# Kernel optimization log

Measured on AMD Instinct MI355X. Metric: run time of the kernel, lower is better.

## Reference

```python
import jax, jax.numpy as jnp
import numpy as np

B, L, E, H = 8192, 64, 128, 8  # batch, max seq len, info_size, head_num
HD = E // H                    # head dim


def setup_inputs() -> dict:
    key = jax.random.key(0)
    k1, k2, k3, k4, k5, k6 = jax.random.split(key, 6)
    inter_info = jax.random.normal(k1, (B, L, E), dtype=jnp.float32)
    # ragged lengths in [1, L] (each sample has at least the query vector)
    lengths = jax.random.randint(k2, (B,), 1, L + 1, dtype=jnp.int32)
    s = 1.0 / np.sqrt(E)
    in_proj_w = jax.random.uniform(k3, (3 * E, E), dtype=jnp.float32, minval=-s, maxval=s)
    in_proj_b = jnp.zeros((3 * E,), dtype=jnp.float32)
    out_proj_w = jax.random.uniform(k4, (E, E), dtype=jnp.float32, minval=-s, maxval=s)
    out_proj_b = jnp.zeros((E,), dtype=jnp.float32)
    return {"inter_info": inter_info, "lengths": lengths,
            "in_proj_w": in_proj_w, "in_proj_b": in_proj_b,
            "out_proj_w": out_proj_w, "out_proj_b": out_proj_b}


def reference(inter_info, lengths, in_proj_w, in_proj_b, out_proj_w, out_proj_b):
    # Per sample: query = first vector, keys/values = all (valid) vectors.
    # Equivalent to torch nn.MultiheadAttention with 1 query per sample.
    Wq, Wk, Wv = in_proj_w[:E], in_proj_w[E:2 * E], in_proj_w[2 * E:]
    bq, bk, bv = in_proj_b[:E], in_proj_b[E:2 * E], in_proj_b[2 * E:]

    query_info = inter_info[:, 0]                                  # [B, E]
    q = (query_info @ Wq.T + bq).reshape(B, H, HD)                 # [B, H, hd]
    k = (inter_info @ Wk.T + bk).reshape(B, L, H, HD)              # [B, L, H, hd]
    v = (inter_info @ Wv.T + bv).reshape(B, L, H, HD)

    scores = jnp.einsum('bhd,blhd->bhl', q, k) / np.sqrt(HD)       # [B, H, L]
    valid = jnp.arange(L)[None, :] < lengths[:, None]              # [B, L]
    scores = jnp.where(valid[:, None, :], scores, -jnp.inf)
    attn = jax.nn.softmax(scores, axis=-1)                         # [B, H, L]

    ctx = jnp.einsum('bhl,blhd->bhd', attn, v).reshape(B, E)       # [B, E]
    attn_hidden = ctx @ out_proj_w.T + out_proj_b                  # [B, E]
    return attn_hidden, query_info
```

## Files before the change

### kernel.cpp

```cpp
#include <hip/hip_runtime.h>
#include <hip/hip_bf16.h>


typedef unsigned int  u32;
typedef unsigned short u16;
typedef unsigned long long u64;

#define XR  136
#define XR4 17
#define YR  136
#define UR  136
#define SCR 68
#define QR  132
#define YSR 1032

#define WS_U_OFF 0u
#define WS_C_OFF 16777216u
#define WS_Y_OFF 17825792u
#define WS_NEED  34603008u

typedef __attribute__((ext_vector_type(8))) __bf16 bf16x8;
typedef __attribute__((ext_vector_type(4))) float  f32x4;

__device__ __forceinline__ float blo(u32 u) { return __uint_as_float(u << 16); }
__device__ __forceinline__ float bhi(u32 u) { return __uint_as_float(u & 0xffff0000u); }
__device__ __forceinline__ float b2f(u16 u) { return __uint_as_float(((u32)u) << 16); }
__device__ __forceinline__ u16 f2b(float f) {
  union { __hip_bfloat16 h; u16 u; } cv; cv.h = __float2bfloat16(f); return cv.u;
}
__device__ __forceinline__ u32 pack2(float a, float b) {
  return (u32)f2b(a) | ((u32)f2b(b) << 16);
}

template<bool BF>
__device__ __forceinline__ uint4 wfrag(const void* p, size_t off) {
  if (BF) {
    return *(const uint4*)((const u16*)p + off);
  } else {
    const float4* q4 = (const float4*)((const float*)p + off);
    float4 a = q4[0], b = q4[1];
    uint4 v;
    v.x = pack2(a.x, a.y); v.y = pack2(a.z, a.w);
    v.z = pack2(b.x, b.y); v.w = pack2(b.z, b.w);
    return v;
  }
}
template<bool BF>
__device__ __forceinline__ void load4(const void* p, size_t off, float* o) {
  if (BF) {
    uint2 v = *(const uint2*)((const u16*)p + off);
    o[0]=blo(v.x); o[1]=bhi(v.x); o[2]=blo(v.y); o[3]=bhi(v.y);
  } else {
    float4 v = *(const float4*)((const float*)p + off);
    o[0]=v.x; o[1]=v.y; o[2]=v.z; o[3]=v.w;
  }
}
template<bool BF>
__device__ __forceinline__ float lds1(const void* p, size_t off) {
  return BF ? b2f(((const u16*)p)[off]) : ((const float*)p)[off];
}

struct __align__(16) SmemK1 {
  u16   X0s[8 * XR];
  float q[8 * QR];
  int   isbf;
};

template<bool BF>
__device__ __forceinline__ void k1_body(SmemK1& S, int b0, int t,
    const void* inter, const void* w_in, const void* b_in,
    u16* Uws, float* Cws)
{
  const int lane = t & 63, w = t >> 6;

  if (t < 128) {
    const int i = t >> 4, ci = t & 15;
    const size_t bidx = (size_t)(b0 + i);
    uint4 v;
    if (BF) {
      v = ((const uint4*)inter)[bidx * 1024 + ci];
    } else {
      const float4* src = (const float4*)inter + bidx * 2048 + ci * 2;
      float4 a = src[0], b = src[1];
      v.x = pack2(a.x, a.y); v.y = pack2(a.z, a.w);
      v.z = pack2(b.x, b.y); v.w = pack2(b.z, b.w);
    }
    *(uint4*)&S.X0s[i * XR + ci * 8] = v;
  }
  __syncthreads();

  {
    const int r15 = lane & 15, e = w * 16 + r15;
    const int kb = (lane >> 4) * 8, rbase = (lane >> 4) * 4;
    f32x4 acc = {0.f, 0.f, 0.f, 0.f};
#pragma unroll
    for (int kc = 0; kc < 4; ++kc) {
      union { uint4 u4; bf16x8 b8; } A, Bf;
      A.u4  = *(const uint4*)&S.X0s[(r15 & 7) * XR + kc * 32 + kb];
      Bf.u4 = wfrag<BF>(w_in, (size_t)e * 128 + kc * 32 + kb);
      acc = __builtin_amdgcn_mfma_f32_16x16x32_bf16(A.b8, Bf.b8, acc, 0, 0, 0);
    }
    const float bq  = lds1<BF>(b_in, e);
    const float bkv = lds1<BF>(b_in, 128 + e);
    float cs[4];
#pragma unroll
    for (int r = 0; r < 4; ++r) {
      float qv = acc[r] + bq;
      if (rbase < 8) S.q[(rbase + r) * QR + e] = qv;
      cs[r] = qv * bkv;
    }
#pragma unroll
    for (int off = 1; off < 16; off <<= 1) {
      cs[0] += __shfl_xor(cs[0], off, 64);
      cs[1] += __shfl_xor(cs[1], off, 64);
      cs[2] += __shfl_xor(cs[2], off, 64);
      cs[3] += __shfl_xor(cs[3], off, 64);
    }
    if (r15 == 0 && rbase < 8) {
#pragma unroll
      for (int r = 0; r < 4; ++r)
        Cws[(size_t)(b0 + rbase + r) * 8 + w] = cs[r];
    }
  }
  __syncthreads();

  {
    const int h = t >> 6, rem = t & 63;
    const int cc = rem >> 1, s = rem & 1;
    float a[4][4] = {{0.f,0.f,0.f,0.f},{0.f,0.f,0.f,0.f},
                     {0.f,0.f,0.f,0.f},{0.f,0.f,0.f,0.f}};
#pragma unroll
    for (int d = 0; d < 16; ++d) {
      float w4[4]; load4<BF>(w_in, (size_t)(128 + h * 16 + d) * 128 + cc * 4, w4);
#pragma unroll
      for (int bi = 0; bi < 4; ++bi) {
        float q0 = S.q[(s * 4 + bi) * QR + h * 16 + d];
        a[bi][0] = fmaf(w4[0], q0, a[bi][0]);
        a[bi][1] = fmaf(w4[1], q0, a[bi][1]);
        a[bi][2] = fmaf(w4[2], q0, a[bi][2]);
        a[bi][3] = fmaf(w4[3], q0, a[bi][3]);
      }
    }
#pragma unroll
    for (int bi = 0; bi < 4; ++bi) {
      const int bt = s * 4 + bi;
      *(uint2*)&Uws[(size_t)(b0 + bt) * 1024 + h * 128 + cc * 4] =
          make_uint2(pack2(a[bi][0], a[bi][1]), pack2(a[bi][2], a[bi][3]));
    }
  }
}

__global__ __launch_bounds__(512, 4) void k1_kernel(
    const void* inter, const void* w_in, const void* b_in,
    u16* Uws, float* Cws)
{
  __shared__ SmemK1 S;
  const int t = threadIdx.x;
  const int b0 = blockIdx.x * 8;
  if (t < 64) {
    float v = b2f(((const u16*)inter)[t]);
    bool bad = !(fabsf(v) < 1000.f);
    u64 m = __ballot(bad);
    if (t == 0) S.isbf = (m == 0ull) ? 1 : 0;
  }
  __syncthreads();
  if (S.isbf) k1_body<true >(S, b0, t, inter, w_in, b_in, Uws, Cws);
  else        k1_body<false>(S, b0, t, inter, w_in, b_in, Uws, Cws);
}

struct __align__(16) SmemK2 {
  u16   Xs[64 * XR];
  u16   u[8 * UR];
  float sc[8][SCR];
  float c[8];
  int   isbf;
};

template<bool BF>
__device__ __forceinline__ void k2_body(SmemK2& S, int b, int t,
    const void* inter, const int* lengths, const u16* Uws, const float* Cws,
    u16* Yws, void* out)
{
  const int len = lengths[b];
  const int lane = t & 63, w = t >> 6;

#pragma unroll
  for (int r = 0; r < 4; ++r) {
    int g = t + 256 * r;
    int l = g >> 4, ci = g & 15;
    uint4 v = make_uint4(0u, 0u, 0u, 0u);
    if (l < len) {
      if (BF) {
        v = ((const uint4*)inter)[(size_t)b * 1024 + g];
        if (l == 0)
          ((uint4*)out)[131072 + (size_t)b * 16 + ci] = v;
      } else {
        const float4* src = (const float4*)inter + (size_t)b * 2048;
        float4 a = src[g * 2], bb = src[g * 2 + 1];
        if (l == 0) {
          float4* o4 = (float4*)out + 262144 + (size_t)b * 32 + ci * 2;
          o4[0] = a; o4[1] = bb;
        }
        v.x = pack2(a.x, a.y); v.y = pack2(a.z, a.w);
        v.z = pack2(bb.x, bb.y); v.w = pack2(bb.z, bb.w);
      }
    }
    ((uint4*)S.Xs)[l * XR4 + ci] = v;
  }
  if (t < 128) {
    const int h = t >> 4, ci = t & 15;
    uint4 v = ((const uint4*)Uws)[(size_t)b * 128 + h * 16 + ci];
    *(uint4*)&S.u[h * UR + ci * 8] = v;
  } else if (t < 136) {
    const int h = t - 128;
    S.c[h] = Cws[(size_t)b * 8 + h];
  }
  __syncthreads();

  if (w * 16 < len) {
    const int arow = w * 16 + (lane & 15);
    const int col  = lane & 15;
    const int kb   = (lane >> 4) * 8;
    const bool hv  = (col < 8);
    f32x4 acc = {0.f, 0.f, 0.f, 0.f};
#pragma unroll
    for (int kc = 0; kc < 4; ++kc) {
      union { uint4 u4; bf16x8 b8; } a, bu;
      a.u4  = *(const uint4*)&S.Xs[arow * XR + kc * 32 + kb];
      bu.u4 = *(const uint4*)&S.u[(col & 7) * UR + kc * 32 + kb];
      if (!hv) bu.u4 = make_uint4(0u, 0u, 0u, 0u);
      acc = __builtin_amdgcn_mfma_f32_16x16x32_bf16(a.b8, bu.b8, acc, 0, 0, 0);
    }
    if (hv) {
      const int l0 = w * 16 + (lane >> 4) * 4;
      const float cadd = S.c[col];
      f32x4 o;
      o[0] = (acc[0] + cadd) * 0.25f;
      o[1] = (acc[1] + cadd) * 0.25f;
      o[2] = (acc[2] + cadd) * 0.25f;
      o[3] = (acc[3] + cadd) * 0.25f;
      *(f32x4*)&S.sc[col][l0] = o;
    }
  }
  __syncthreads();

  {
    const int h = t >> 5, sub = t & 31;
    const int l0 = sub, l1 = sub + 32;
    float s0 = S.sc[h][l0], s1 = S.sc[h][l1];
    const bool v0 = l0 < len, v1 = l1 < len;
    float m = fmaxf(v0 ? s0 : -INFINITY, v1 ? s1 : -INFINITY);
#pragma unroll
    for (int off = 16; off > 0; off >>= 1) m = fmaxf(m, __shfl_xor(m, off, 32));
    float e0 = v0 ? __expf(s0 - m) : 0.f;
    float e1 = v1 ? __expf(s1 - m) : 0.f;
    float s = e0 + e1;
#pragma unroll
    for (int off = 16; off > 0; off >>= 1) s += __shfl_xor(s, off, 32);
    float inv = 1.f / s;
    S.sc[h][l0] = e0 * inv;
    S.sc[h][l1] = e1 * inv;
  }
  __syncthreads();

  {
    const int j0 = w * 32;
    const int hA = (lane & 15) < 8 ? (lane & 15) : 7;
    const int l8 = (lane >> 4) * 8;
    const int jc0 = j0 + (lane & 15), jc1 = jc0 + 16;
    f32x4 acc0 = {0.f,0.f,0.f,0.f}, acc1 = {0.f,0.f,0.f,0.f};
    const u16* xb = S.Xs;
    {
      const int lb = l8;
      float4 pa = *(const float4*)&S.sc[hA][lb];
      float4 pb = *(const float4*)&S.sc[hA][lb + 4];
      union { u32 u[4]; bf16x8 b; } A, B0, B1;
      A.u[0] = pack2(pa.x, pa.y); A.u[1] = pack2(pa.z, pa.w);
      A.u[2] = pack2(pb.x, pb.y); A.u[3] = pack2(pb.z, pb.w);
#pragma unroll
      for (int jj = 0; jj < 4; ++jj) {
        u32 lo0 = xb[(lb+2*jj)*XR + jc0], hi0 = xb[(lb+2*jj+1)*XR + jc0];
        u32 lo1 = xb[(lb+2*jj)*XR + jc1], hi1 = xb[(lb+2*jj+1)*XR + jc1];
        B0.u[jj] = lo0 | (hi0 << 16);
        B1.u[jj] = lo1 | (hi1 << 16);
      }
      acc0 = __builtin_amdgcn_mfma_f32_16x16x32_bf16(A.b, B0.b, acc0, 0, 0, 0);
      acc1 = __builtin_amdgcn_mfma_f32_16x16x32_bf16(A.b, B1.b, acc1, 0, 0, 0);
    }
    if (len > 32) {
      const int lb = 32 + l8;
      float4 pa = *(const float4*)&S.sc[hA][lb];
      float4 pb = *(const float4*)&S.sc[hA][lb + 4];
      union { u32 u[4]; bf16x8 b; } A, B0, B1;
      A.u[0] = pack2(pa.x, pa.y); A.u[1] = pack2(pa.z, pa.w);
      A.u[2] = pack2(pb.x, pb.y); A.u[3] = pack2(pb.z, pb.w);
#pragma unroll
      for (int jj = 0; jj < 4; ++jj) {
        u32 lo0 = xb[(lb+2*jj)*XR + jc0], hi0 = xb[(lb+2*jj+1)*XR + jc0];
        u32 lo1 = xb[(lb+2*jj)*XR + jc1], hi1 = xb[(lb+2*jj+1)*XR + jc1];
        B0.u[jj] = lo0 | (hi0 << 16);
        B1.u[jj] = lo1 | (hi1 << 16);
      }
      acc0 = __builtin_amdgcn_mfma_f32_16x16x32_bf16(A.b, B0.b, acc0, 0, 0, 0);
      acc1 = __builtin_amdgcn_mfma_f32_16x16x32_bf16(A.b, B1.b, acc1, 0, 0, 0);
    }
    const int rbase = (lane >> 4) * 4;
    if (rbase < 8) {
      u16* yo = Yws + (size_t)b * 1024;
#pragma unroll
      for (int r = 0; r < 4; ++r) {
        yo[(rbase + r) * 128 + j0 + (lane & 15)]      = f2b(acc0[r]);
        yo[(rbase + r) * 128 + j0 + 16 + (lane & 15)] = f2b(acc1[r]);
      }
    }
  }
}

__global__ __launch_bounds__(256, 4) void k2_kernel(
    const void* inter, const int* __restrict__ lengths,
    const u16* Uws, const float* Cws, u16* Yws, void* out)
{
  __shared__ SmemK2 S;
  const int t = threadIdx.x;
  const int b = blockIdx.x;
  if (t < 64) {
    float v = b2f(((const u16*)inter)[t]);
    bool bad = !(fabsf(v) < 1000.f);
    u64 m = __ballot(bad);
    if (t == 0) S.isbf = (m == 0ull) ? 1 : 0;
  }
  __syncthreads();
  if (S.isbf) k2_body<true >(S, b, t, inter, lengths, Uws, Cws, Yws, out);
  else        k2_body<false>(S, b, t, inter, lengths, Uws, Cws, Yws, out);
}

struct __align__(16) SmemK3 {
  u16 ys[16 * YSR];
  u16 ctx[16 * 136];
  int isbf;
};

template<bool BF>
__device__ __forceinline__ void k3_body(SmemK3& S, int b0, int t,
    const u16* Yws, const void* w_in, const void* b_in,
    const void* w_out, const void* b_out, void* out)
{
  const int lane = t & 63, w = t >> 6;

#pragma unroll
  for (int r = 0; r < 4; ++r) {
    int idx = t + 512 * r;
    int row = idx >> 7, ci = idx & 127;
    uint4 v = ((const uint4*)Yws)[(size_t)(b0 + row) * 128 + ci];
    *(uint4*)&S.ys[row * YSR + ci * 8] = v;
  }
  __syncthreads();

  {
    const int col = lane & 15, kb = (lane >> 4) * 8, rbase = (lane >> 4) * 4;
    f32x4 acc = {0.f, 0.f, 0.f, 0.f};
#pragma unroll
    for (int kc = 0; kc < 4; ++kc) {
      union { uint4 u4; bf16x8 b8; } A, Bf;
      A.u4  = *(const uint4*)&S.ys[col * YSR + w * 128 + kc * 32 + kb];
      Bf.u4 = wfrag<BF>(w_in, (size_t)(256 + w * 16 + col) * 128 + kc * 32 + kb);
      acc = __builtin_amdgcn_mfma_f32_16x16x32_bf16(A.b8, Bf.b8, acc, 0, 0, 0);
    }
    const float bv = lds1<BF>(b_in, 256 + w * 16 + col);
#pragma unroll
    for (int r = 0; r < 4; ++r)
      S.ctx[(rbase + r) * 136 + w * 16 + col] = f2b(acc[r] + bv);
  }
  __syncthreads();

  {
    const int col = lane & 15, kb = (lane >> 4) * 8, rbase = (lane >> 4) * 4;
    f32x4 acc = {0.f, 0.f, 0.f, 0.f};
#pragma unroll
    for (int kc = 0; kc < 4; ++kc) {
      union { uint4 u4; bf16x8 b8; } A, Bf;
      A.u4  = *(const uint4*)&S.ctx[col * 136 + kc * 32 + kb];
      Bf.u4 = wfrag<BF>(w_out, (size_t)(w * 16 + col) * 128 + kc * 32 + kb);
      acc = __builtin_amdgcn_mfma_f32_16x16x32_bf16(A.b8, Bf.b8, acc, 0, 0, 0);
    }
    const float bo = lds1<BF>(b_out, w * 16 + col);
#pragma unroll
    for (int r = 0; r < 4; ++r) {
      float v = acc[r] + bo;
      size_t oo = (size_t)(b0 + rbase + r) * 128 + w * 16 + col;
      if (BF) ((u16*)out)[oo] = f2b(v);
      else    ((float*)out)[oo] = v;
    }
  }
}

__global__ __launch_bounds__(512, 4) void k3_kernel(
    const u16* Yws, const void* w_in, const void* b_in,
    const void* w_out, const void* b_out, void* out)
{
  __shared__ SmemK3 S;
  const int t = threadIdx.x;
  const int b0 = blockIdx.x * 16;
  if (t < 64) {
    float v = b2f(((const u16*)w_out)[t]);
    bool bad = !(fabsf(v) < 1000.f);
    u64 m = __ballot(bad);
    if (t == 0) S.isbf = (m == 0ull) ? 1 : 0;
  }
  __syncthreads();
  if (S.isbf) k3_body<true >(S, b0, t, Yws, w_in, b_in, w_out, b_out, out);
  else        k3_body<false>(S, b0, t, Yws, w_in, b_in, w_out, b_out, out);
}

struct __align__(16) SmemM {
  u16   Xs[2][64 * XR];
  u16   u[2][8 * UR];
  u16   y[2][8 * YR];
  float q[2][128];
  float sc[2][8][SCR];
  float c[2][8];
  float ctx[2][128];
  int   isbf;
};

template<bool BF>
__device__ __forceinline__ void mono_body(SmemM& S, int b0, int t,
    const void* inter, const int* lengths, const void* w_in, const void* b_in,
    const void* w_out, const void* b_out, void* out)
{
  const int len0 = lengths[b0];
  const int len1 = lengths[b0 + 1];
  const int lane = t & 63, w = t >> 6;

#pragma unroll
  for (int r = 0; r < 4; ++r) {
    int g = t + 512 * r;
    int tile = g >> 10, gg = g & 1023, l = gg >> 4, ci = gg & 15;
    uint4 v = make_uint4(0u, 0u, 0u, 0u);
    if (l < (tile ? len1 : len0)) {
      if (BF) {
        v = ((const uint4*)inter)[(size_t)b0 * 1024 + g];
      } else {
        const float4* src = (const float4*)inter + (size_t)b0 * 2048;
        float4 a = src[g * 2], b = src[g * 2 + 1];
        v.x = pack2(a.x, a.y); v.y = pack2(a.z, a.w);
        v.z = pack2(b.x, b.y); v.w = pack2(b.z, b.w);
      }
    }
    ((uint4*)S.Xs[tile])[l * XR4 + ci] = v;
  }
  __syncthreads();

  {
    const int e = w * 16 + (lane & 15);
    const int btc = (lane & 15) < 2 ? (lane & 15) : 1;
    const int kb = (lane >> 4) * 8;
    f32x4 acc = {0.f, 0.f, 0.f, 0.f};
#pragma unroll
    for (int kc = 0; kc < 4; ++kc) {
      union { uint4 u4; bf16x8 b8; } A, Bf;
      A.u4  = *(const uint4*)&S.Xs[btc][kc * 32 + kb];
      Bf.u4 = wfrag<BF>(w_in, (size_t)e * 128 + kc * 32 + kb);
      acc = __builtin_amdgcn_mfma_f32_16x16x32_bf16(A.b8, Bf.b8, acc, 0, 0, 0);
    }
    if (lane < 16) {
      float bq = lds1<BF>(b_in, e);
      S.q[0][e] = acc[0] + bq;
      S.q[1][e] = acc[1] + bq;
    }
  }
  __syncthreads();

  {
    const int bt = t >> 8, h = (t >> 5) & 7, cc = t & 31;
    float a0=0.f,a1=0.f,a2=0.f,a3=0.f;
#pragma unroll
    for (int d = 0; d < 16; ++d) {
      float w4[4]; load4<BF>(w_in, (size_t)(128 + h * 16 + d) * 128 + cc * 4, w4);
      float q0 = S.q[bt][h * 16 + d];
      a0 = fmaf(w4[0], q0, a0); a1 = fmaf(w4[1], q0, a1);
      a2 = fmaf(w4[2], q0, a2); a3 = fmaf(w4[3], q0, a3);
    }
    *(uint2*)&S.u[bt][h * UR + cc * 4] = make_uint2(pack2(a0, a1), pack2(a2, a3));
    if (cc == 0) {
      float c0 = 0.f;
      for (int d = 0; d < 16; ++d)
        c0 += S.q[bt][h * 16 + d] * lds1<BF>(b_in, 128 + h * 16 + d);
      S.c[bt][h] = c0;
    }
  }
  __syncthreads();

  {
    const int bt = w >> 2, mt = w & 3;
    const int arow = mt * 16 + (lane & 15);
    const int col  = lane & 15;
    const int kb   = (lane >> 4) * 8;
    const bool hv  = (col < 8);
    f32x4 acc = {0.f, 0.f, 0.f, 0.f};
#pragma unroll
    for (int kc = 0; kc < 4; ++kc) {
      union { uint4 u4; bf16x8 b8; } a, bu;
      a.u4  = *(const uint4*)&S.Xs[bt][arow * XR + kc * 32 + kb];
      bu.u4 = *(const uint4*)&S.u[bt][(col & 7) * UR + kc * 32 + kb];
      if (!hv) bu.u4 = make_uint4(0u, 0u, 0u, 0u);
      acc = __builtin_amdgcn_mfma_f32_16x16x32_bf16(a.b8, bu.b8, acc, 0, 0, 0);
    }
    if (hv) {
      const int l0 = mt * 16 + (lane >> 4) * 4;
      const float cadd = S.c[bt][col];
      f32x4 o;
      o[0] = (acc[0] + cadd) * 0.25f;
      o[1] = (acc[1] + cadd) * 0.25f;
      o[2] = (acc[2] + cadd) * 0.25f;
      o[3] = (acc[3] + cadd) * 0.25f;
      *(f32x4*)&S.sc[bt][col][l0] = o;
    }
  }
  __syncthreads();

  {
    const int bt = t >> 8, h = (t >> 5) & 7, sub = t & 31;
    const int len = bt ? len1 : len0;
    const int l0 = sub, l1 = sub + 32;
    float s0 = S.sc[bt][h][l0], s1 = S.sc[bt][h][l1];
    const bool v0 = l0 < len, v1 = l1 < len;
    float m = fmaxf(v0 ? s0 : -INFINITY, v1 ? s1 : -INFINITY);
#pragma unroll
    for (int off = 16; off > 0; off >>= 1) m = fmaxf(m, __shfl_xor(m, off, 32));
    float e0 = v0 ? __expf(s0 - m) : 0.f;
    float e1 = v1 ? __expf(s1 - m) : 0.f;
    float s = e0 + e1;
#pragma unroll
    for (int off = 16; off > 0; off >>= 1) s += __shfl_xor(s, off, 32);
    float inv = 1.f / s;
    S.sc[bt][h][l0] = e0 * inv;
    S.sc[bt][h][l1] = e1 * inv;
  }
  __syncthreads();

  {
    const int bt = w >> 2, j0 = (w & 3) * 32;
    const int hA = (lane & 15) < 8 ? (lane & 15) : 7;
    const int l8 = (lane >> 4) * 8;
    const int jc0 = j0 + (lane & 15), jc1 = jc0 + 16;
    const int len = bt ? len1 : len0;
    f32x4 acc0 = {0.f,0.f,0.f,0.f}, acc1 = {0.f,0.f,0.f,0.f};
    const u16* xb = S.Xs[bt];
    {
      const int lb = l8;
      float4 pa = *(const float4*)&S.sc[bt][hA][lb];
      float4 pb = *(const float4*)&S.sc[bt][hA][lb + 4];
      union { u32 u[4]; bf16x8 b; } A, B0, B1;
      A.u[0] = pack2(pa.x, pa.y); A.u[1] = pack2(pa.z, pa.w);
      A.u[2] = pack2(pb.x, pb.y); A.u[3] = pack2(pb.z, pb.w);
#pragma unroll
      for (int jj = 0; jj < 4; ++jj) {
        u32 lo0 = xb[(lb+2*jj)*XR + jc0], hi0 = xb[(lb+2*jj+1)*XR + jc0];
        u32 lo1 = xb[(lb+2*jj)*XR + jc1], hi1 = xb[(lb+2*jj+1)*XR + jc1];
        B0.u[jj] = lo0 | (hi0 << 16);
        B1.u[jj] = lo1 | (hi1 << 16);
      }
      acc0 = __builtin_amdgcn_mfma_f32_16x16x32_bf16(A.b, B0.b, acc0, 0, 0, 0);
      acc1 = __builtin_amdgcn_mfma_f32_16x16x32_bf16(A.b, B1.b, acc1, 0, 0, 0);
    }
    if (len > 32) {
      const int lb = 32 + l8;
      float4 pa = *(const float4*)&S.sc[bt][hA][lb];
      float4 pb = *(const float4*)&S.sc[bt][hA][lb + 4];
      union { u32 u[4]; bf16x8 b; } A, B0, B1;
      A.u[0] = pack2(pa.x, pa.y); A.u[1] = pack2(pa.z, pa.w);
      A.u[2] = pack2(pb.x, pb.y); A.u[3] = pack2(pb.z, pb.w);
#pragma unroll
      for (int jj = 0; jj < 4; ++jj) {
        u32 lo0 = xb[(lb+2*jj)*XR + jc0], hi0 = xb[(lb+2*jj+1)*XR + jc0];
        u32 lo1 = xb[(lb+2*jj)*XR + jc1], hi1 = xb[(lb+2*jj+1)*XR + jc1];
        B0.u[jj] = lo0 | (hi0 << 16);
        B1.u[jj] = lo1 | (hi1 << 16);
      }
      acc0 = __builtin_amdgcn_mfma_f32_16x16x32_bf16(A.b, B0.b, acc0, 0, 0, 0);
      acc1 = __builtin_amdgcn_mfma_f32_16x16x32_bf16(A.b, B1.b, acc1, 0, 0, 0);
    }
    const int rbase = (lane >> 4) * 4;
    if (rbase < 8) {
#pragma unroll
      for (int r = 0; r < 4; ++r) {
        S.y[bt][(rbase + r) * YR + j0 + (lane & 15)]      = f2b(acc0[r]);
        S.y[bt][(rbase + r) * YR + j0 + 16 + (lane & 15)] = f2b(acc1[r]);
      }
    }
  }
  __syncthreads();

  {
    const int e = w * 16 + (lane & 15);
    const int btc = (lane & 15) < 2 ? (lane & 15) : 1;
    const int kb = (lane >> 4) * 8;
    f32x4 acc = {0.f, 0.f, 0.f, 0.f};
#pragma unroll
    for (int kc = 0; kc < 4; ++kc) {
      union { uint4 u4; bf16x8 b8; } A, Bf;
      A.u4  = *(const uint4*)&S.y[btc][w * YR + kc * 32 + kb];
      Bf.u4 = wfrag<BF>(w_in, (size_t)(256 + e) * 128 + kc * 32 + kb);
      acc = __builtin_amdgcn_mfma_f32_16x16x32_bf16(A.b8, Bf.b8, acc, 0, 0, 0);
    }
    if (lane < 16) {
      S.ctx[0][e] = acc[0] + lds1<BF>(b_in, 256 + e);
      S.ctx[1][e] = acc[1] + lds1<BF>(b_in, 256 + e);
    }
  }
  __syncthreads();

  {
    const int e = w * 16 + (lane & 15);
    const int btc = (lane & 15) < 2 ? (lane & 15) : 1;
    const int kb = (lane >> 4) * 8;
    f32x4 acc = {0.f, 0.f, 0.f, 0.f};
#pragma unroll
    for (int kc = 0; kc < 4; ++kc) {
      union { u32 u[4]; bf16x8 b; } A;
      union { uint4 u4; bf16x8 b8; } Bf;
      float4 ca = *(const float4*)&S.ctx[btc][kc * 32 + kb];
      float4 cb = *(const float4*)&S.ctx[btc][kc * 32 + kb + 4];
      A.u[0] = pack2(ca.x, ca.y); A.u[1] = pack2(ca.z, ca.w);
      A.u[2] = pack2(cb.x, cb.y); A.u[3] = pack2(cb.z, cb.w);
      Bf.u4 = wfrag<BF>(w_out, (size_t)e * 128 + kc * 32 + kb);
      acc = __builtin_amdgcn_mfma_f32_16x16x32_bf16(A.b, Bf.b8, acc, 0, 0, 0);
    }
    if (lane < 16) {
      float bo = lds1<BF>(b_out, e);
      float a0 = acc[0] + bo, a1 = acc[1] + bo;
      if (BF) {
        ((u16*)out)[(size_t)b0 * 128 + e]       = f2b(a0);
        ((u16*)out)[(size_t)(b0 + 1) * 128 + e] = f2b(a1);
      } else {
        ((float*)out)[(size_t)b0 * 128 + e]       = a0;
        ((float*)out)[(size_t)(b0 + 1) * 128 + e] = a1;
      }
    } else if (lane < 48) {
      const int bt = (lane >> 4) - 1;
      size_t o1 = (size_t)8192 * 128 + (size_t)(b0 + bt) * 128 + e;
      u16 xv = S.Xs[bt][e];
      if (BF) ((u16*)out)[o1] = xv;
      else    ((float*)out)[o1] = b2f(xv);
    }
  }
}

__global__ __launch_bounds__(512, 4) void mono_kernel(
    const void* inter, const int* __restrict__ lengths,
    const void* w_in, const void* b_in, const void* w_out, const void* b_out,
    void* out)
{
  __shared__ SmemM S;
  const int t = threadIdx.x;
  const int b0 = blockIdx.x * 2;
  if (t < 64) {
    float v = b2f(((const u16*)inter)[t]);
    bool bad = !(fabsf(v) < 1000.f);
    u64 m = __ballot(bad);
    if (t == 0) S.isbf = (m == 0ull) ? 1 : 0;
  }
  __syncthreads();
  if (S.isbf) mono_body<true >(S, b0, t, inter, lengths, w_in, b_in, w_out, b_out, out);
  else        mono_body<false>(S, b0, t, inter, lengths, w_in, b_in, w_out, b_out, out);
}

extern "C" void kernel_launch(void* const* d_in, const int* in_sizes, int n_in,
                              void* d_out, int out_size, void* d_ws, size_t ws_size,
                              hipStream_t stream) {
  if (d_ws && ws_size >= (size_t)WS_NEED) {
    u16*   Uws = (u16*)((char*)d_ws + WS_U_OFF);
    float* Cws = (float*)((char*)d_ws + WS_C_OFF);
    u16*   Yws = (u16*)((char*)d_ws + WS_Y_OFF);
    k1_kernel<<<dim3(1024), dim3(512), 0, stream>>>(
        d_in[0], d_in[2], d_in[3], Uws, Cws);
    k2_kernel<<<dim3(8192), dim3(256), 0, stream>>>(
        d_in[0], (const int*)d_in[1], Uws, Cws, Yws, d_out);
    k3_kernel<<<dim3(512), dim3(512), 0, stream>>>(
        Yws, d_in[2], d_in[3], d_in[4], d_in[5], d_out);
  } else {
    mono_kernel<<<dim3(4096), dim3(512), 0, stream>>>(
        d_in[0], (const int*)d_in[1], d_in[2], d_in[3], d_in[4], d_in[5], d_out);
  }
}
```

Before: 368.7 us.

## Store inter_info transposed in LDS as packed bf16 pairs; read score A-operand from global

The k2 kernel now stages the per-sample input in LDS transposed, with two consecutive sequence positions packed into one 32-bit word per feature. The P·X MFMA B-operand can then be read as whole words instead of gathered from scattered 16-bit loads. The score MFMA now reads its A-operand straight from global memory (L1/L2 hits) instead of from the old row-major LDS copy. This cuts LDS gather instructions and bank conflicts, at the cost of strided transposed LDS writes and repeated global reads. For fp32 inputs it also adds repeated bf16 conversion.

```diff
diff --git a/kernel.cpp b/kernel.cpp
--- a/kernel.cpp
+++ b/kernel.cpp
@@ -13,6 +13,7 @@
 #define SCR 68
 #define QR  132
 #define YSR 1032
+#define XTR 33
 
 #define WS_U_OFF 0u
 #define WS_C_OFF 16777216u
@@ -169,7 +170,7 @@
 }
 
 struct __align__(16) SmemK2 {
-  u16   Xs[64 * XR];
+  u32   xT[128 * XTR];
   u16   u[8 * UR];
   float sc[8][SCR];
   float c[8];
@@ -184,28 +185,47 @@
   const int len = lengths[b];
   const int lane = t & 63, w = t >> 6;
 
-#pragma unroll
-  for (int r = 0; r < 4; ++r) {
-    int g = t + 256 * r;
-    int l = g >> 4, ci = g & 15;
-    uint4 v = make_uint4(0u, 0u, 0u, 0u);
-    if (l < len) {
+  {
+    const int ci = t & 15, lp0 = t >> 4;
+#pragma unroll
+    for (int r = 0; r < 2; ++r) {
+      const int lp = lp0 + 16 * r;
+      const int la = 2 * lp, lb = 2 * lp + 1;
       if (BF) {
-        v = ((const uint4*)inter)[(size_t)b * 1024 + g];
-        if (l == 0)
-          ((uint4*)out)[131072 + (size_t)b * 16 + ci] = v;
+        uint4 va = make_uint4(0u,0u,0u,0u), vb = make_uint4(0u,0u,0u,0u);
+        const uint4* src = (const uint4*)inter + (size_t)b * 1024;
+        if (la < len) va = src[la * 16 + ci];
+        if (lb < len) vb = src[lb * 16 + ci];
+        if (lp == 0)
+          ((uint4*)out)[131072 + (size_t)b * 16 + ci] = va;
+        const u32* pa = (const u32*)&va;
+        const u32* pb = (const u32*)&vb;
+#pragma unroll
+        for (int jw = 0; jw < 4; ++jw) {
+          u32 wa = pa[jw], wb = pb[jw];
+          S.xT[(ci * 8 + jw * 2)     * XTR + lp] = (wa & 0xffffu)  | (wb << 16);
+          S.xT[(ci * 8 + jw * 2 + 1) * XTR + lp] = (wa >> 16) | (wb & 0xffff0000u);
+        }
       } else {
+        float4 fa0 = {0,0,0,0}, fa1 = {0,0,0,0}, fb0 = {0,0,0,0}, fb1 = {0,0,0,0};
         const float4* src = (const float4*)inter + (size_t)b * 2048;
-        float4 a = src[g * 2], bb = src[g * 2 + 1];
-        if (l == 0) {
+        if (la < len) { fa0 = src[(la * 16 + ci) * 2]; fa1 = src[(la * 16 + ci) * 2 + 1]; }
+        if (lb < len) { fb0 = src[(lb * 16 + ci) * 2]; fb1 = src[(lb * 16 + ci) * 2 + 1]; }
+        if (lp == 0) {
           float4* o4 = (float4*)out + 262144 + (size_t)b * 32 + ci * 2;
-          o4[0] = a; o4[1] = bb;
+          o4[0] = fa0; o4[1] = fa1;
         }
-        v.x = pack2(a.x, a.y); v.y = pack2(a.z, a.w);
-        v.z = pack2(bb.x, bb.y); v.w = pack2(bb.z, bb.w);
-      }
-    }
-    ((uint4*)S.Xs)[l * XR4 + ci] = v;
+        const int r0 = ci * 8;
+        S.xT[(r0 + 0) * XTR + lp] = pack2(fa0.x, fb0.x);
+        S.xT[(r0 + 1) * XTR + lp] = pack2(fa0.y, fb0.y);
+        S.xT[(r0 + 2) * XTR + lp] = pack2(fa0.z, fb0.z);
+        S.xT[(r0 + 3) * XTR + lp] = pack2(fa0.w, fb0.w);
+        S.xT[(r0 + 4) * XTR + lp] = pack2(fa1.x, fb1.x);
+        S.xT[(r0 + 5) * XTR + lp] = pack2(fa1.y, fb1.y);
+        S.xT[(r0 + 6) * XTR + lp] = pack2(fa1.z, fb1.z);
+        S.xT[(r0 + 7) * XTR + lp] = pack2(fa1.w, fb1.w);
+      }
+    }
   }
   if (t < 128) {
     const int h = t >> 4, ci = t & 15;
@@ -226,7 +246,16 @@
 #pragma unroll
     for (int kc = 0; kc < 4; ++kc) {
       union { uint4 u4; bf16x8 b8; } a, bu;
-      a.u4  = *(const uint4*)&S.Xs[arow * XR + kc * 32 + kb];
+      if (BF) {
+        a.u4 = *(const uint4*)((const u16*)inter +
+                 (size_t)b * 8192 + (size_t)arow * 128 + kc * 32 + kb);
+      } else {
+        const float4* xf = (const float4*)((const float*)inter +
+                 (size_t)b * 8192 + (size_t)arow * 128 + kc * 32 + kb);
+        float4 x0 = xf[0], x1 = xf[1];
+        a.u4 = make_uint4(pack2(x0.x, x0.y), pack2(x0.z, x0.w),
+                          pack2(x1.x, x1.y), pack2(x1.z, x1.w));
+      }
       bu.u4 = *(const uint4*)&S.u[(col & 7) * UR + kc * 32 + kb];
       if (!hv) bu.u4 = make_uint4(0u, 0u, 0u, 0u);
       acc = __builtin_amdgcn_mfma_f32_16x16x32_bf16(a.b8, bu.b8, acc, 0, 0, 0);
@@ -269,9 +298,24 @@
     const int l8 = (lane >> 4) * 8;
     const int jc0 = j0 + (lane & 15), jc1 = jc0 + 16;
     f32x4 acc0 = {0.f,0.f,0.f,0.f}, acc1 = {0.f,0.f,0.f,0.f};
-    const u16* xb = S.Xs;
     {
-      const int lb = l8;
+      const int lpb = l8 >> 1;
+      float4 pa = *(const float4*)&S.sc[hA][l8];
+      float4 pb = *(const float4*)&S.sc[hA][l8 + 4];
+      union { u32 u[4]; bf16x8 b; } A, B0, B1;
+      A.u[0] = pack2(pa.x, pa.y); A.u[1] = pack2(pa.z, pa.w);
+      A.u[2] = pack2(pb.x, pb.y); A.u[3] = pack2(pb.z, pb.w);
+#pragma unroll
+      for (int jj = 0; jj < 4; ++jj) {
+        B0.u[jj] = S.xT[jc0 * XTR + lpb + jj];
+        B1.u[jj] = S.xT[jc1 * XTR + lpb + jj];
+      }
+      acc0 = __builtin_amdgcn_mfma_f32_16x16x32_bf16(A.b, B0.b, acc0, 0, 0, 0);
+      acc1 = __builtin_amdgcn_mfma_f32_16x16x32_bf16(A.b, B1.b, acc1, 0, 0, 0);
+    }
+    if (len > 32) {
+      const int lb = 32 + l8;
+      const int lpb = lb >> 1;
       float4 pa = *(const float4*)&S.sc[hA][lb];
       float4 pb = *(const float4*)&S.sc[hA][lb + 4];
       union { u32 u[4]; bf16x8 b; } A, B0, B1;
@@ -279,27 +323,8 @@
       A.u[2] = pack2(pb.x, pb.y); A.u[3] = pack2(pb.z, pb.w);
 #pragma unroll
       for (int jj = 0; jj < 4; ++jj) {
-        u32 lo0 = xb[(lb+2*jj)*XR + jc0], hi0 = xb[(lb+2*jj+1)*XR + jc0];
-        u32 lo1 = xb[(lb+2*jj)*XR + jc1], hi1 = xb[(lb+2*jj+1)*XR + jc1];
-        B0.u[jj] = lo0 | (hi0 << 16);
-        B1.u[jj] = lo1 | (hi1 << 16);
-      }
-      acc0 = __builtin_amdgcn_mfma_f32_16x16x32_bf16(A.b, B0.b, acc0, 0, 0, 0);
-      acc1 = __builtin_amdgcn_mfma_f32_16x16x32_bf16(A.b, B1.b, acc1, 0, 0, 0);
-    }
-    if (len > 32) {
-      const int lb = 32 + l8;
-      float4 pa = *(const float4*)&S.sc[hA][lb];
-      float4 pb = *(const float4*)&S.sc[hA][lb + 4];
-      union { u32 u[4]; bf16x8 b; } A, B0, B1;
-      A.u[0] = pack2(pa.x, pa.y); A.u[1] = pack2(pa.z, pa.w);
-      A.u[2] = pack2(pb.x, pb.y); A.u[3] = pack2(pb.z, pb.w);
-#pragma unroll
-      for (int jj = 0; jj < 4; ++jj) {
-        u32 lo0 = xb[(lb+2*jj)*XR + jc0], hi0 = xb[(lb+2*jj+1)*XR + jc0];
-        u32 lo1 = xb[(lb+2*jj)*XR + jc1], hi1 = xb[(lb+2*jj+1)*XR + jc1];
-        B0.u[jj] = lo0 | (hi0 << 16);
-        B1.u[jj] = lo1 | (hi1 << 16);
+        B0.u[jj] = S.xT[jc0 * XTR + lpb + jj];
+        B1.u[jj] = S.xT[jc1 * XTR + lpb + jj];
       }
       acc0 = __builtin_amdgcn_mfma_f32_16x16x32_bf16(A.b, B0.b, acc0, 0, 0, 0);
       acc1 = __builtin_amdgcn_mfma_f32_16x16x32_bf16(A.b, B1.b, acc1, 0, 0, 0);
```

New measurement: 375.2 us. Within noise of the previous version (+1.8%).
